# Kernel optimization log

Measured on AMD Instinct MI355X. Metric: run time of the kernel, lower is better.

Reference implementation:

```python
import jax, jax.numpy as jnp
import numpy as np

EPS = 1e-7  # K.epsilon()

def setup_inputs() -> dict:
    key = jax.random.key(0)
    k1, k2, k3 = jax.random.split(key, 3)
    B, T, D = 32, 2048, 512
    x = jax.random.normal(k1, (B, T, D), dtype=jnp.float32)
    W = jax.random.normal(k2, (D, D), dtype=jnp.float32) * (1.0 / np.sqrt(D))
    b = jnp.zeros((D,), dtype=jnp.float32)
    u = jax.random.normal(k3, (D,), dtype=jnp.float32) * (1.0 / np.sqrt(D))
    return {"x": x, "W": W, "b": b, "u": u}

def reference(x, W, b, u):
    # uit = tanh(x @ W + b)  -> [B, T, D]
    uit = jnp.tanh(jnp.einsum('btd,de->bte', x, W) + b)
    # scores: sum over feature dim of uit * u -> [B, T]
    ait = jnp.einsum('btd,d->bt', uit, u)
    # exp + normalize over T (no mask); matches original exp/sum form
    a = jnp.exp(ait)
    a = a / (jnp.sum(a, axis=1, keepdims=True) + EPS)
    # weighted sum pooling over T -> [B, D]
    return jnp.einsum('btd,bt->bd', x, a)
```

## Files before the change

### kernel.cpp

```cpp
#include <hip/hip_runtime.h>
#include <math.h>

#define D_DIM 512

typedef short short8v __attribute__((ext_vector_type(8)));
typedef unsigned short ushort8v __attribute__((ext_vector_type(8)));
typedef unsigned short ushort4v __attribute__((ext_vector_type(4)));
typedef float f32x16 __attribute__((ext_vector_type(16)));

__device__ inline unsigned short f2bf(float f) {
    union { float f; unsigned int u; } a; a.f = f;
    unsigned int u = a.u;
    unsigned int r = (u + 0x7fffu + ((u >> 16) & 1u)) >> 16;
    return (unsigned short)r;
}

__device__ inline float fast_tanh(float y) {
    float e2 = __expf(2.f * y);
    return 1.f - __fdividef(2.f, e2 + 1.f);
}

#define ASYNC_CP16(gp, lp) \
    __builtin_amdgcn_global_load_lds( \
        (const __attribute__((address_space(1))) void*)(gp), \
        (__attribute__((address_space(3))) void*)(lp), 16, 0, 0)

__global__ __launch_bounds__(1024) void wt_kernel(const float* __restrict__ W,
                                                  unsigned short* __restrict__ Wb2) {
    __shared__ __align__(16) unsigned short lbuf[16384];
    const int s = blockIdx.x;
    const int tid = threadIdx.x;
    #pragma unroll
    for (int i = 0; i < 4; ++i) {
        int flat = tid + i * 1024;
        int kr = flat >> 7;
        int e4 = (flat & 127) * 4;
        float4 v = *(const float4*)(W + (size_t)(s * 32 + kr) * D_DIM + e4);
        int ks = kr >> 4, half = (kr >> 3) & 1, j = kr & 7;
        float vv[4] = {v.x, v.y, v.z, v.w};
        #pragma unroll
        for (int q = 0; q < 4; ++q) {
            int e = e4 + q, nt = e >> 5, nl = e & 31;
            lbuf[(((nt * 2 + ks) * 2 + half) * 32 + nl) * 8 + j] = f2bf(vv[q]);
        }
    }
    __syncthreads();
    #pragma unroll
    for (int i = 0; i < 2; ++i) {
        int c = tid + i * 1024;
        *(ushort8v*)(Wb2 + (size_t)s * 16384 + c * 8) = *(const ushort8v*)&lbuf[c * 8];
    }
}

constexpr int XLDE = 40;

__global__ __launch_bounds__(512, 4) void gemm_ait_mfma(
    const float* __restrict__ x, const unsigned short* __restrict__ Wb2,
    const float* __restrict__ bias, const float* __restrict__ u,
    float* __restrict__ ait)
{
    __shared__ __align__(16) unsigned short wsh[2][16384];
    __shared__ __align__(16) unsigned short xs[2][64 * XLDE];
    __shared__ float rowpart[8][64];

    const int tid  = threadIdx.x;
    const int wave = tid >> 6;
    const int lane = tid & 63;
    const int half = lane >> 5;
    const int nl   = lane & 31;
    const int m0   = blockIdx.x * 64;

    f32x16 acc[2][2];
    #pragma unroll
    for (int mi = 0; mi < 2; ++mi)
        #pragma unroll
        for (int ni = 0; ni < 2; ++ni)
            #pragma unroll
            for (int r = 0; r < 16; ++r) acc[mi][ni][r] = 0.f;

    const int xr  = tid >> 3;
    const int xc4 = tid & 7;
    const float* xbase = x + (size_t)(m0 + xr) * D_DIM + xc4 * 4;

    #pragma unroll
    for (int i = 0; i < 4; ++i)
        ASYNC_CP16(Wb2 + tid * 8 + i * 4096, &wsh[0][tid * 8 + i * 4096]);
    float4 px = *(const float4*)(xbase);

    for (int s = 0; s < 16; ++s) {
        const int pb = s & 1;
        {
            ushort4v pk;
            pk[0] = f2bf(px.x); pk[1] = f2bf(px.y);
            pk[2] = f2bf(px.z); pk[3] = f2bf(px.w);
            *(ushort4v*)&xs[pb][xr * XLDE + xc4 * 4] = pk;
        }
        __syncthreads();

        if (s + 1 < 16) {
            const unsigned short* wsrc = Wb2 + (size_t)(s + 1) * 16384;
            #pragma unroll
            for (int i = 0; i < 4; ++i)
                ASYNC_CP16(wsrc + tid * 8 + i * 4096, &wsh[1 - pb][tid * 8 + i * 4096]);
            px = *(const float4*)(xbase + (s + 1) * 32);
        }

        #pragma unroll
        for (int ks = 0; ks < 2; ++ks) {
            short8v af[2], bfr[2];
            #pragma unroll
            for (int mi = 0; mi < 2; ++mi)
                af[mi] = *(const short8v*)&xs[pb][(mi * 32 + nl) * XLDE + ks * 16 + half * 8];
            #pragma unroll
            for (int ni = 0; ni < 2; ++ni)
                bfr[ni] = *(const short8v*)&wsh[pb][(((wave * 2 + ni) * 2 + ks) * 2 + half) * 256 + nl * 8];
            #pragma unroll
            for (int mi = 0; mi < 2; ++mi)
                #pragma unroll
                for (int ni = 0; ni < 2; ++ni)
                    acc[mi][ni] = __builtin_amdgcn_mfma_f32_32x32x16_bf16(
                        af[mi], bfr[ni], acc[mi][ni], 0, 0, 0);
        }
    }

    float rowsum[2][16];
    #pragma unroll
    for (int mi = 0; mi < 2; ++mi)
        #pragma unroll
        for (int r = 0; r < 16; ++r) rowsum[mi][r] = 0.f;

    #pragma unroll
    for (int mi = 0; mi < 2; ++mi) {
        #pragma unroll
        for (int ni = 0; ni < 2; ++ni) {
            int col = wave * 64 + ni * 32 + nl;
            float be = bias[col], ue = u[col];
            #pragma unroll
            for (int r = 0; r < 16; ++r)
                rowsum[mi][r] += fast_tanh(acc[mi][ni][r] + be) * ue;
        }
    }
    #pragma unroll
    for (int mi = 0; mi < 2; ++mi)
        #pragma unroll
        for (int r = 0; r < 16; ++r) {
            float v = rowsum[mi][r];
            v += __shfl_xor(v, 1, 64);
            v += __shfl_xor(v, 2, 64);
            v += __shfl_xor(v, 4, 64);
            v += __shfl_xor(v, 8, 64);
            v += __shfl_xor(v, 16, 64);
            rowsum[mi][r] = v;
        }
    if (nl == 0) {
        #pragma unroll
        for (int mi = 0; mi < 2; ++mi)
            #pragma unroll
            for (int r = 0; r < 16; ++r) {
                int row = mi * 32 + (r & 3) + 8 * (r >> 2) + 4 * half;
                rowpart[wave][row] = rowsum[mi][r];
            }
    }
    __syncthreads();
    if (tid < 64) {
        float s = 0.f;
        #pragma unroll
        for (int w = 0; w < 8; ++w) s += rowpart[w][tid];
        ait[m0 + tid] = s;
    }
}

__global__ __launch_bounds__(256) void gemm_ait_f32(
    const float* __restrict__ x, const float* __restrict__ W,
    const float* __restrict__ bias, const float* __restrict__ u,
    float* __restrict__ ait)
{
    __shared__ float xsf[64][68];
    __shared__ float wshf[64][132];
    const int tid = threadIdx.x;
    const int tx = tid & 15, ty = tid >> 4;
    const int m0 = blockIdx.x * 64;
    float rowsum[4] = {0.f, 0.f, 0.f, 0.f};
    for (int e0 = 0; e0 < D_DIM; e0 += 128) {
        float acc[4][8];
        #pragma unroll
        for (int i = 0; i < 4; ++i)
            #pragma unroll
            for (int j = 0; j < 8; ++j) acc[i][j] = 0.f;
        for (int kc = 0; kc < D_DIM; kc += 64) {
            #pragma unroll
            for (int i = 0; i < 4; ++i) {
                int idx = tid + i * 256;
                int r = idx >> 4, c = (idx & 15) * 4;
                *(float4*)&xsf[r][c] = *(const float4*)(x + (size_t)(m0 + r) * D_DIM + kc + c);
            }
            #pragma unroll
            for (int i = 0; i < 8; ++i) {
                int idx = tid + i * 256;
                int r = idx >> 5, c = (idx & 31) * 4;
                *(float4*)&wshf[r][c] = *(const float4*)(W + (size_t)(kc + r) * D_DIM + e0 + c);
            }
            __syncthreads();
            #pragma unroll 4
            for (int k = 0; k < 64; ++k) {
                float xv[4];
                #pragma unroll
                for (int i = 0; i < 4; ++i) xv[i] = xsf[ty * 4 + i][k];
                float4 w0 = *(const float4*)&wshf[k][tx * 8];
                float4 w1 = *(const float4*)&wshf[k][tx * 8 + 4];
                #pragma unroll
                for (int i = 0; i < 4; ++i) {
                    acc[i][0] += xv[i] * w0.x; acc[i][1] += xv[i] * w0.y;
                    acc[i][2] += xv[i] * w0.z; acc[i][3] += xv[i] * w0.w;
                    acc[i][4] += xv[i] * w1.x; acc[i][5] += xv[i] * w1.y;
                    acc[i][6] += xv[i] * w1.z; acc[i][7] += xv[i] * w1.w;
                }
            }
            __syncthreads();
        }
        #pragma unroll
        for (int j = 0; j < 8; ++j) {
            int e = e0 + tx * 8 + j;
            float be = bias[e], ue = u[e];
            #pragma unroll
            for (int i = 0; i < 4; ++i) rowsum[i] += tanhf(acc[i][j] + be) * ue;
        }
    }
    float* red = &xsf[0][0];
    #pragma unroll
    for (int i = 0; i < 4; ++i) red[(ty * 4 + i) * 16 + tx] = rowsum[i];
    __syncthreads();
    if (tid < 64) {
        float s = 0.f;
        #pragma unroll
        for (int j = 0; j < 16; ++j) s += red[tid * 16 + j];
        ait[m0 + tid] = s;
    }
}

__global__ __launch_bounds__(256) void softmax_kernel(float* __restrict__ ait, int T)
{
    const int b = blockIdx.x;
    float* p = ait + (size_t)b * T;
    const int tid = threadIdx.x;
    float ev[8];
    float local = 0.f;
    #pragma unroll
    for (int i = 0; i < 8; ++i) {
        ev[i] = expf(p[tid + i * 256]);
        local += ev[i];
    }
    #pragma unroll
    for (int off = 32; off > 0; off >>= 1)
        local += __shfl_down(local, off, 64);
    __shared__ float wsum[4];
    const int wv = tid >> 6, lane = tid & 63;
    if (lane == 0) wsum[wv] = local;
    __syncthreads();
    float total = wsum[0] + wsum[1] + wsum[2] + wsum[3];
    float inv = 1.0f / (total + 1e-7f);
    #pragma unroll
    for (int i = 0; i < 8; ++i) p[tid + i * 256] = ev[i] * inv;
}

__global__ __launch_bounds__(512) void pool_partial_kernel(
    const float* __restrict__ x, const float* __restrict__ a,
    float* __restrict__ partial, int T)
{
    const int chunks = T >> 8;
    const int b = blockIdx.x / chunks;
    const int c = blockIdx.x % chunks;
    const int tid = threadIdx.x;
    const int th = tid >> 7;
    const int d = (tid & 127) * 4;

    const float* xp = x + ((size_t)b * T + c * 256) * D_DIM + d;
    const float* ap = a + (size_t)b * T + c * 256;

    float4 acc = {0.f, 0.f, 0.f, 0.f};
    #pragma unroll 8
    for (int t = th; t < 256; t += 4) {
        float s = ap[t];
        float4 xv = *(const float4*)(xp + (size_t)t * D_DIM);
        acc.x += xv.x * s; acc.y += xv.y * s;
        acc.z += xv.z * s; acc.w += xv.w * s;
    }
    __shared__ float4 tmp[3][128];
    if (th > 0) tmp[th - 1][tid & 127] = acc;
    __syncthreads();
    if (th == 0) {
        float4 o0 = tmp[0][tid], o1 = tmp[1][tid], o2 = tmp[2][tid];
        acc.x += o0.x + o1.x + o2.x; acc.y += o0.y + o1.y + o2.y;
        acc.z += o0.z + o1.z + o2.z; acc.w += o0.w + o1.w + o2.w;
        *(float4*)(partial + (size_t)blockIdx.x * D_DIM + tid * 4) = acc;
    }
}

__global__ __launch_bounds__(256) void pool_reduce_kernel(
    const float* __restrict__ partial, float* __restrict__ out, int chunks)
{
    const int b = blockIdx.x;
    const int tid = threadIdx.x;
    const int d = tid * 2;
    float2 acc = {0.f, 0.f};
    for (int c = 0; c < chunks; ++c) {
        float2 v = *(const float2*)(partial + ((size_t)b * chunks + c) * D_DIM + d);
        acc.x += v.x; acc.y += v.y;
    }
    *(float2*)(out + (size_t)b * D_DIM + d) = acc;
}

__global__ __launch_bounds__(256) void pool_atomic_kernel(
    const float* __restrict__ x, const float* __restrict__ a,
    float* __restrict__ out, int T)
{
    const int chunks = T >> 8;
    const int b = blockIdx.x / chunks;
    const int c = blockIdx.x % chunks;
    const int tid = threadIdx.x;
    const int th = tid >> 7;
    const int d = (tid & 127) * 4;
    const float* xp = x + ((size_t)b * T + c * 256) * D_DIM + d;
    const float* ap = a + (size_t)b * T + c * 256;
    float4 acc = {0.f, 0.f, 0.f, 0.f};
    #pragma unroll 8
    for (int t = th; t < 256; t += 2) {
        float s = ap[t];
        float4 xv = *(const float4*)(xp + (size_t)t * D_DIM);
        acc.x += xv.x * s; acc.y += xv.y * s;
        acc.z += xv.z * s; acc.w += xv.w * s;
    }
    __shared__ float4 tmp[128];
    if (th == 1) tmp[tid & 127] = acc;
    __syncthreads();
    if (th == 0) {
        float4 o = tmp[tid];
        float* op = out + (size_t)b * D_DIM + tid * 4;
        atomicAdd(op + 0, acc.x + o.x);
        atomicAdd(op + 1, acc.y + o.y);
        atomicAdd(op + 2, acc.z + o.z);
        atomicAdd(op + 3, acc.w + o.w);
    }
}

extern "C" void kernel_launch(void* const* d_in, const int* in_sizes, int n_in,
                              void* d_out, int out_size, void* d_ws, size_t ws_size,
                              hipStream_t stream)
{
    const float* x    = (const float*)d_in[0];
    const float* W    = (const float*)d_in[1];
    const float* bias = (const float*)d_in[2];
    const float* u    = (const float*)d_in[3];
    float* out = (float*)d_out;

    const int Dd = in_sizes[2];
    const int M  = in_sizes[0] / Dd;
    const int B  = out_size / Dd;
    const int T  = M / B;
    const int chunks = T >> 8;

    const size_t wb_bytes  = (size_t)Dd * Dd * sizeof(unsigned short);
    const size_t ait_bytes = (size_t)M * sizeof(float);

    if (ws_size >= wb_bytes + ait_bytes) {
        unsigned short* Wb2 = (unsigned short*)d_ws;
        float* ait     = (float*)((char*)d_ws + wb_bytes);
        float* partial = (float*)d_ws;

        wt_kernel<<<dim3(16), dim3(1024), 0, stream>>>(W, Wb2);
        gemm_ait_mfma<<<dim3(M / 64), dim3(512), 0, stream>>>(x, Wb2, bias, u, ait);
        softmax_kernel<<<dim3(B), dim3(256), 0, stream>>>(ait, T);
        pool_partial_kernel<<<dim3(B * chunks), dim3(512), 0, stream>>>(x, ait, partial, T);
        pool_reduce_kernel<<<dim3(B), dim3(256), 0, stream>>>(partial, out, chunks);
    } else {
        float* ait = (float*)d_ws;
        gemm_ait_f32<<<dim3(M / 64), dim3(256), 0, stream>>>(x, W, bias, u, ait);
        softmax_kernel<<<dim3(B), dim3(256), 0, stream>>>(ait, T);
        hipMemsetAsync(d_out, 0, (size_t)out_size * sizeof(float), stream);
        pool_atomic_kernel<<<dim3(B * chunks), dim3(256), 0, stream>>>(x, ait, out, T);
    }
}
```

Baseline: 256.6 us.

## Fuse softmax and weighted pooling into GEMM epilogue with atomic accumulation

The GEMM kernel now exponentiates its row scores and, while the x tile is likely still in cache, accumulates the exp-weighted sum of x into a per-batch numerator, with atomic adds for both the numerator and the denominator. A small final kernel divides the numerator by the denominator. This drops the separate softmax, pool-partial and reduce kernels and the second full read of x from HBM. In exchange it adds float atomics (non-deterministic summation order), skips max-subtraction just as the reference does, and makes the weight-convert kernel zero the accumulators.

```diff
diff --git a/kernel.cpp b/kernel.cpp
--- a/kernel.cpp
+++ b/kernel.cpp
@@ -26,10 +26,15 @@
         (__attribute__((address_space(3))) void*)(lp), 16, 0, 0)
 
 __global__ __launch_bounds__(1024) void wt_kernel(const float* __restrict__ W,
-                                                  unsigned short* __restrict__ Wb2) {
+                                                  unsigned short* __restrict__ Wb2,
+                                                  float* __restrict__ zero_base,
+                                                  int zero_count) {
     __shared__ __align__(16) unsigned short lbuf[16384];
     const int s = blockIdx.x;
     const int tid = threadIdx.x;
+    if (s == 0) {
+        for (int i = tid; i < zero_count; i += 1024) zero_base[i] = 0.f;
+    }
     #pragma unroll
     for (int i = 0; i < 4; ++i) {
         int flat = tid + i * 1024;
@@ -54,10 +59,10 @@
 
 constexpr int XLDE = 40;
 
-__global__ __launch_bounds__(512, 4) void gemm_ait_mfma(
+__global__ __launch_bounds__(512, 4) void gemm_ait_fused(
     const float* __restrict__ x, const unsigned short* __restrict__ Wb2,
     const float* __restrict__ bias, const float* __restrict__ u,
-    float* __restrict__ ait)
+    float* __restrict__ numer, float* __restrict__ denom, int T)
 {
     __shared__ __align__(16) unsigned short wsh[2][16384];
     __shared__ __align__(16) unsigned short xs[2][64 * XLDE];
@@ -162,12 +167,60 @@
             }
     }
     __syncthreads();
+
+    const int b = m0 / T;
+    float* evals = (float*)&xs[0][0];
     if (tid < 64) {
         float s = 0.f;
         #pragma unroll
         for (int w = 0; w < 8; ++w) s += rowpart[w][tid];
-        ait[m0 + tid] = s;
-    }
+        float e = __expf(s);
+        evals[tid] = e;
+        float t = e;
+        t += __shfl_xor(t, 1, 64);
+        t += __shfl_xor(t, 2, 64);
+        t += __shfl_xor(t, 4, 64);
+        t += __shfl_xor(t, 8, 64);
+        t += __shfl_xor(t, 16, 64);
+        t += __shfl_xor(t, 32, 64);
+        if (tid == 0) atomicAdd(denom + b, t);
+    }
+    __syncthreads();
+
+    const int dg = tid >> 7;
+    const int d4 = (tid & 127) << 2;
+    const float* xp = x + (size_t)m0 * D_DIM + d4;
+    float4 pacc = {0.f, 0.f, 0.f, 0.f};
+    #pragma unroll 4
+    for (int r = dg; r < 64; r += 4) {
+        float e = evals[r];
+        float4 xv = *(const float4*)(xp + (size_t)r * D_DIM);
+        pacc.x += e * xv.x; pacc.y += e * xv.y;
+        pacc.z += e * xv.z; pacc.w += e * xv.w;
+    }
+    float4* ptmp = (float4*)&wsh[0][0];
+    if (dg > 0) ptmp[(dg - 1) * 128 + (tid & 127)] = pacc;
+    __syncthreads();
+    if (dg == 0) {
+        float4 o0 = ptmp[tid], o1 = ptmp[128 + tid], o2 = ptmp[256 + tid];
+        float* np = numer + (size_t)b * D_DIM + d4;
+        atomicAdd(np + 0, pacc.x + o0.x + o1.x + o2.x);
+        atomicAdd(np + 1, pacc.y + o0.y + o1.y + o2.y);
+        atomicAdd(np + 2, pacc.z + o0.z + o1.z + o2.z);
+        atomicAdd(np + 3, pacc.w + o0.w + o1.w + o2.w);
+    }
+}
+
+__global__ __launch_bounds__(128) void out_div_kernel(
+    const float* __restrict__ numer, const float* __restrict__ denom,
+    float* __restrict__ out)
+{
+    const int b = blockIdx.x;
+    const int tid = threadIdx.x;
+    float inv = 1.0f / (denom[b] + 1e-7f);
+    float4 v = *(const float4*)(numer + (size_t)b * D_DIM + tid * 4);
+    v.x *= inv; v.y *= inv; v.z *= inv; v.w *= inv;
+    *(float4*)(out + (size_t)b * D_DIM + tid * 4) = v;
 }
 
 __global__ __launch_bounds__(256) void gemm_ait_f32(
@@ -263,53 +316,6 @@
     for (int i = 0; i < 8; ++i) p[tid + i * 256] = ev[i] * inv;
 }
 
-__global__ __launch_bounds__(512) void pool_partial_kernel(
-    const float* __restrict__ x, const float* __restrict__ a,
-    float* __restrict__ partial, int T)
-{
-    const int chunks = T >> 8;
-    const int b = blockIdx.x / chunks;
-    const int c = blockIdx.x % chunks;
-    const int tid = threadIdx.x;
-    const int th = tid >> 7;
-    const int d = (tid & 127) * 4;
-
-    const float* xp = x + ((size_t)b * T + c * 256) * D_DIM + d;
-    const float* ap = a + (size_t)b * T + c * 256;
-
-    float4 acc = {0.f, 0.f, 0.f, 0.f};
-    #pragma unroll 8
-    for (int t = th; t < 256; t += 4) {
-        float s = ap[t];
-        float4 xv = *(const float4*)(xp + (size_t)t * D_DIM);
-        acc.x += xv.x * s; acc.y += xv.y * s;
-        acc.z += xv.z * s; acc.w += xv.w * s;
-    }
-    __shared__ float4 tmp[3][128];
-    if (th > 0) tmp[th - 1][tid & 127] = acc;
-    __syncthreads();
-    if (th == 0) {
-        float4 o0 = tmp[0][tid], o1 = tmp[1][tid], o2 = tmp[2][tid];
-        acc.x += o0.x + o1.x + o2.x; acc.y += o0.y + o1.y + o2.y;
-        acc.z += o0.z + o1.z + o2.z; acc.w += o0.w + o1.w + o2.w;
-        *(float4*)(partial + (size_t)blockIdx.x * D_DIM + tid * 4) = acc;
-    }
-}
-
-__global__ __launch_bounds__(256) void pool_reduce_kernel(
-    const float* __restrict__ partial, float* __restrict__ out, int chunks)
-{
-    const int b = blockIdx.x;
-    const int tid = threadIdx.x;
-    const int d = tid * 2;
-    float2 acc = {0.f, 0.f};
-    for (int c = 0; c < chunks; ++c) {
-        float2 v = *(const float2*)(partial + ((size_t)b * chunks + c) * D_DIM + d);
-        acc.x += v.x; acc.y += v.y;
-    }
-    *(float2*)(out + (size_t)b * D_DIM + d) = acc;
-}
-
 __global__ __launch_bounds__(256) void pool_atomic_kernel(
     const float* __restrict__ x, const float* __restrict__ a,
     float* __restrict__ out, int T)
@@ -364,14 +370,14 @@
 
     if (ws_size >= wb_bytes + ait_bytes) {
         unsigned short* Wb2 = (unsigned short*)d_ws;
-        float* ait     = (float*)((char*)d_ws + wb_bytes);
-        float* partial = (float*)d_ws;
-
-        wt_kernel<<<dim3(16), dim3(1024), 0, stream>>>(W, Wb2);
-        gemm_ait_mfma<<<dim3(M / 64), dim3(512), 0, stream>>>(x, Wb2, bias, u, ait);
-        softmax_kernel<<<dim3(B), dim3(256), 0, stream>>>(ait, T);
-        pool_partial_kernel<<<dim3(B * chunks), dim3(512), 0, stream>>>(x, ait, partial, T);
-        pool_reduce_kernel<<<dim3(B), dim3(256), 0, stream>>>(partial, out, chunks);
+        float* numer = (float*)((char*)d_ws + wb_bytes);
+        float* denom = numer + (size_t)B * Dd;
+        const int zero_count = B * Dd + B;
+
+        wt_kernel<<<dim3(16), dim3(1024), 0, stream>>>(W, Wb2, numer, zero_count);
+        gemm_ait_fused<<<dim3(M / 64), dim3(512), 0, stream>>>(x, Wb2, bias, u,
+                                                               numer, denom, T);
+        out_div_kernel<<<dim3(B), dim3(128), 0, stream>>>(numer, denom, out);
     } else {
         float* ait = (float*)d_ws;
         gemm_ait_f32<<<dim3(M / 64), dim3(256), 0, stream>>>(x, W, bias, u, ait);
```

Measured after the change: 242.1 us. 5.7% less time.
